# Performance work log

Hardware: AMD Instinct MI355X
Metric: run time of the kernel (lower is better)

## Reference

```python
import jax, jax.numpy as jnp
import numpy as np

S = 15      # subject_nums
C = 2048    # in_channels (extractor output dim)
NC = 3      # num_classes
B = 1024    # subject_batch_num (rows per subject)
SUBJ = 7    # target subject
KERNEL_MUL = 2.0
KERNEL_NUM = 5


def setup_inputs() -> dict:
    key = jax.random.key(0)
    k = jax.random.split(key, 5)
    x = jax.random.normal(k[0], (S * B, C), dtype=jnp.float32)
    labels = jax.random.randint(k[1], (S * B,), 0, NC)
    y = jax.nn.one_hot(labels, NC, dtype=jnp.float32)
    subject_label = jnp.repeat(jnp.arange(S, dtype=jnp.int32), B)
    W_add = 0.02 * jax.random.normal(k[2], (S, 512, C), dtype=jnp.float32)
    b_add = jnp.zeros((S, 512), dtype=jnp.float32)
    W_cls = 0.02 * jax.random.normal(k[3], (S, NC, 512), dtype=jnp.float32)
    b_cls = jnp.zeros((S, NC), dtype=jnp.float32)
    return {"x": x, "y": y, "subject_label": subject_label,
            "W_add": W_add, "b_add": b_add, "W_cls": W_cls, "b_cls": b_cls,
            "subject": SUBJ}


def _mmd(source, target):
    # Standard multi-kernel Gaussian MMD (DAN-style), as used in the repo.
    n = source.shape[0]
    total = jnp.concatenate([source, target], axis=0)      # [2n, d]
    sq = jnp.sum(total * total, axis=-1)
    d2 = sq[:, None] + sq[None, :] - 2.0 * (total @ total.T)  # [2n, 2n]
    m = 2 * n
    bandwidth = jnp.sum(d2) / (m * m - m)
    bandwidth = bandwidth / (KERNEL_MUL ** (KERNEL_NUM // 2))
    kernels = sum(jnp.exp(-d2 / (bandwidth * (KERNEL_MUL ** i))) for i in range(KERNEL_NUM))
    XX = kernels[:n, :n]
    YY = kernels[n:, n:]
    XY = kernels[:n, n:]
    YX = kernels[n:, :n]
    return jnp.mean(XX + YY - XY - YX)


def reference(x, y, subject_label, W_add, b_add, W_cls, b_cls, subject):
    S_ = W_add.shape[0]
    b = x.shape[0] // S_          # == (subject_label == subject).sum() by construction
    K = S_ - 1
    idx = np.array([i for i in range(S_) if i != subject])  # static: subject is a Python int

    xr = x.reshape(S_, b, -1)
    src = xr[idx]                 # [K, b, C] source-subject blocks
    tgt = xr[subject]             # [b, C] target-subject block
    Wk, bk = W_add[idx], b_add[idx]

    # Grouped per-subject addblock Linear(C -> 512)
    outs = jnp.einsum('kbc,kdc->kbd', src, Wk) + bk[:, None, :]       # [K, b, 512]
    t_outs = jnp.einsum('bc,kdc->kbd', tgt, Wk) + bk[:, None, :]      # [K, b, 512]

    # Class predictors: ReLU + Linear(512 -> NC), predictors 0..K-1 are used
    Wc, bc = W_cls[:K], b_cls[:K]
    logits = jnp.einsum('kbd,knd->kbn', jax.nn.relu(outs), Wc) + bc[:, None, :]
    t_logits = jnp.einsum('kbd,knd->kbn', jax.nn.relu(t_outs), Wc) + bc[:, None, :]

    # ---- MMD loss ----
    mmd_loss = jnp.mean(jax.vmap(_mmd)(outs, t_outs))

    # ---- DISC loss: pairwise |softmax - softmax| over source features ----
    P = jax.nn.softmax(outs, axis=-1)                                  # [K, b, 512]
    disc_loss = 0.0
    for i in range(K - 1):  # fixed small loop over subjects, inner term vectorized
        disc_loss = disc_loss + jnp.abs(P[i + 1:] - P[i]).mean(axis=(1, 2)).sum()
    disc_loss = disc_loss * 2.0 / (K * (K - 1))

    # ---- CLS loss: KL(one-hot/soft target || log_softmax(logits)) ----
    yr = y.reshape(S_, b, -1)[idx]                                     # [K, b, NC]
    logp = jax.nn.log_softmax(logits, axis=-1)
    safe_y = jnp.where(yr > 0, yr, 1.0)
    kl = jnp.where(yr > 0, yr * (jnp.log(safe_y) - logp), 0.0)         # 0*log0 -> 0 (torch kl_div)
    cls_loss = kl.sum(-1).mean()

    # ---- PRED ACC on target subject ----
    t_prob = jax.nn.softmax(t_logits, axis=-1).mean(axis=0)            # [b, NC]
    y_tgt = y.reshape(S_, b, -1)[subject]
    pred = jnp.sum(jnp.argmax(t_prob, axis=1) == jnp.argmax(y_tgt, axis=1))
    nums = b

    return (mmd_loss * 0.1, disc_loss * 0.4, cls_loss, pred, nums)
```

## Files before the change

kernel.cpp:

```cpp
#include <hip/hip_runtime.h>
#include <hip/hip_bf16.h>
#include <stdint.h>

typedef __attribute__((ext_vector_type(8))) __bf16 bf16x8;
typedef __attribute__((ext_vector_type(4))) float f32x4;

#define CDIM 2048
#define DDIM 512

__device__ __forceinline__ unsigned short f2bf(float f) {
  union { float f; unsigned u; } a; a.f = f;
  unsigned r = a.u + 0x7FFFu + ((a.u >> 16) & 1u);
  return (unsigned short)(r >> 16);
}
__device__ __forceinline__ float bf2f(unsigned short h) {
  union { unsigned u; float f; } a; a.u = ((unsigned)h) << 16;
  return a.f;
}

typedef const __attribute__((address_space(1))) void gas_void;
typedef __attribute__((address_space(3))) void las_void;
__device__ __forceinline__ void async16(const void* g, void* l) {
  __builtin_amdgcn_global_load_lds((gas_void*)g, (las_void*)l, 16, 0, 0);
}

__device__ __forceinline__ float blockSum256(float v) {
  __shared__ float sh[4];
  #pragma unroll
  for (int o = 32; o; o >>= 1) v += __shfl_xor(v, o, 64);
  int lane = threadIdx.x & 63, w = threadIdx.x >> 6;
  __syncthreads();
  if (lane == 0) sh[w] = v;
  __syncthreads();
  return sh[0] + sh[1] + sh[2] + sh[3];
}

__device__ __forceinline__ bf16x8 lds_frag(const unsigned short* base, int row, int cb) {
  return *(const bf16x8*)(base + row*64 + (((cb ^ (row & 7))) << 3));
}

__global__ __launch_bounds__(256) void k_convert(const float* __restrict__ x,
    const float* __restrict__ w, uint2* __restrict__ x16, uint2* __restrict__ w16) {
  const int nx4 = 15*1024*CDIM/4;
  const int nw4 = 15*DDIM*CDIM/4;
  int stride = gridDim.x * blockDim.x;
  for (int i = blockIdx.x*blockDim.x + threadIdx.x; i < nx4; i += stride) {
    float4 v = ((const float4*)x)[i];
    x16[i] = make_uint2((unsigned)f2bf(v.x) | ((unsigned)f2bf(v.y) << 16),
                        (unsigned)f2bf(v.z) | ((unsigned)f2bf(v.w) << 16));
  }
  for (int i = blockIdx.x*blockDim.x + threadIdx.x; i < nw4; i += stride) {
    float4 v = ((const float4*)w)[i];
    w16[i] = make_uint2((unsigned)f2bf(v.x) | ((unsigned)f2bf(v.y) << 16),
                        (unsigned)f2bf(v.z) | ((unsigned)f2bf(v.w) << 16));
  }
}

__global__ __launch_bounds__(256) void k_gemm1(
    const unsigned short* __restrict__ x16,
    const unsigned short* __restrict__ w16,
    const float* __restrict__ b_add,
    const int* __restrict__ subj_p,
    unsigned short* __restrict__ t16)
{
  const int subj = *subj_p;
  int bid = blockIdx.x;
  int k  = bid >> 6;
  int t  = bid & 63;
  int mt = t >> 2, nt = t & 3;
  int ik = (k < subj) ? k : (k + 1);

  __shared__ unsigned short As[128*64];
  __shared__ unsigned short Bs[128*64];

  int tid = threadIdx.x;
  int lane = tid & 63;
  int w = tid >> 6;
  int wm = w >> 1, wn = w & 1;
  int rlane = lane >> 3;
  int col8  = ((lane & 7) ^ rlane) << 3;

  const unsigned short* Bbase = w16 + (size_t)ik * DDIM * CDIM;

  f32x4 acc[4][4];
  #pragma unroll
  for (int a = 0; a < 4; a++)
    #pragma unroll
    for (int b = 0; b < 4; b++) acc[a][b] = f32x4{0.f,0.f,0.f,0.f};

  for (int ks = 0; ks < CDIM; ks += 64) {
    #pragma unroll
    for (int i = 0; i < 4; i++) {
      int c = w*4 + i;
      int r = c*8 + rlane;
      int gr = mt*128 + r;
      int xrow = ((gr < 1024) ? ik : subj) * 1024 + (gr & 1023);
      async16(x16 + (size_t)xrow*CDIM + ks + col8, (char*)As + c*1024);
      int gn = nt*128 + r;
      async16(Bbase + (size_t)gn*CDIM + ks + col8, (char*)Bs + c*1024);
    }
    __syncthreads();
    #pragma unroll
    for (int kk = 0; kk < 64; kk += 32) {
      bf16x8 af[4], bfr[4];
      #pragma unroll
      for (int a = 0; a < 4; a++)
        af[a] = lds_frag(As, wm*64 + a*16 + (lane & 15), (kk >> 3) + (lane >> 4));
      #pragma unroll
      for (int b = 0; b < 4; b++)
        bfr[b] = lds_frag(Bs, wn*64 + b*16 + (lane & 15), (kk >> 3) + (lane >> 4));
      #pragma unroll
      for (int a = 0; a < 4; a++)
        #pragma unroll
        for (int b = 0; b < 4; b++)
          acc[a][b] = __builtin_amdgcn_mfma_f32_16x16x32_bf16(af[a], bfr[b], acc[a][b], 0, 0, 0);
    }
    __syncthreads();
  }
  const float* bias = b_add + ik*DDIM;
  #pragma unroll
  for (int b = 0; b < 4; b++) {
    int coln = nt*128 + wn*64 + b*16 + (lane & 15);
    float bv = bias[coln];
    #pragma unroll
    for (int a = 0; a < 4; a++) {
      #pragma unroll
      for (int r = 0; r < 4; r++) {
        int rowm = mt*128 + wm*64 + a*16 + ((lane >> 4) << 2) + r;
        t16[((size_t)k*2048 + rowm)*DDIM + coln] = f2bf(acc[a][b][r] + bv);
      }
    }
  }
}

__global__ __launch_bounds__(256) void k_rowred(const unsigned short* __restrict__ t16,
    float* __restrict__ sq, float* __restrict__ rmax, float* __restrict__ rinv,
    float* __restrict__ scol)
{
  __shared__ float cs[4][512];
  int tidx = threadIdx.x;
  int w = tidx >> 6;
  int lane = tidx & 63;
  int wid = blockIdx.x*4 + w;
  int k = wid >> 11;
  uint4 v = *(const uint4*)(t16 + (size_t)wid * DDIM + lane*8);
  unsigned uu[4] = {v.x, v.y, v.z, v.w};
  float f[8];
  #pragma unroll
  for (int q = 0; q < 4; q++) {
    f[2*q]   = bf2f((unsigned short)(uu[q] & 0xffffu));
    f[2*q+1] = bf2f((unsigned short)(uu[q] >> 16));
  }
  float s2 = 0.f, mx = -3.4e38f;
  #pragma unroll
  for (int j = 0; j < 8; j++) { s2 += f[j]*f[j]; mx = fmaxf(mx, f[j]); }
  #pragma unroll
  for (int o = 32; o; o >>= 1) { s2 += __shfl_xor(s2, o, 64); mx = fmaxf(mx, __shfl_xor(mx, o, 64)); }
  float se = 0.f;
  #pragma unroll
  for (int j = 0; j < 8; j++) se += __expf(f[j] - mx);
  #pragma unroll
  for (int o = 32; o; o >>= 1) se += __shfl_xor(se, o, 64);
  if (lane == 0) { sq[wid] = s2; rmax[wid] = mx; rinv[wid] = 1.f/se; }
  #pragma unroll
  for (int j = 0; j < 8; j++) cs[w][lane*8 + j] = f[j];
  __syncthreads();
  atomicAdd(&scol[k*512 + tidx],       cs[0][tidx]     + cs[1][tidx]     + cs[2][tidx]     + cs[3][tidx]);
  atomicAdd(&scol[k*512 + 256 + tidx], cs[0][tidx+256] + cs[1][tidx+256] + cs[2][tidx+256] + cs[3][tidx+256]);
}

__global__ __launch_bounds__(256) void k_bw(const float* __restrict__ sq,
    const float* __restrict__ scol, float* __restrict__ c2)
{
  int k = blockIdx.x;
  float a = 0.f;
  for (int r = threadIdx.x; r < 2048; r += 256) a += sq[k*2048 + r];
  float b = 0.f;
  for (int d = threadIdx.x; d < 512; d += 256) { float v = scol[k*512 + d]; b += v*v; }
  float atot = blockSum256(a);
  float btot = blockSum256(b);
  if (threadIdx.x == 0) {
    float sumd2 = 2.f*2048.f*atot - 2.f*btot;
    float bw = sumd2 / (2048.f*2048.f - 2048.f) * 0.25f;
    #pragma unroll
    for (int i = 0; i < 5; i++)
      c2[k*5 + i] = -1.4426950408889634f / (bw * (float)(1 << i));
  }
}

__global__ __launch_bounds__(256) void k_mmd(
    const unsigned short* __restrict__ t16,
    const float* __restrict__ sq,
    const float* __restrict__ c2,
    float* __restrict__ g_acc)
{
  int bid = blockIdx.x;
  int k = bid / 136;
  int tri = bid - k*136;
  int it = 0;
  while (tri >= 16 - it) { tri -= 16 - it; it++; }
  int jt = it + tri;

  const unsigned short* T = t16 + (size_t)k * 2048 * DDIM;

  __shared__ unsigned short As[128*64];
  __shared__ unsigned short Bs[128*64];
  __shared__ float sqs[256];

  int tid = threadIdx.x;
  int lane = tid & 63;
  int w = tid >> 6;
  int wm = w >> 1, wn = w & 1;
  int rlane = lane >> 3;
  int col8  = ((lane & 7) ^ rlane) << 3;

  f32x4 acc[4][4];
  #pragma unroll
  for (int a = 0; a < 4; a++)
    #pragma unroll
    for (int b = 0; b < 4; b++) acc[a][b] = f32x4{0.f,0.f,0.f,0.f};

  for (int ks = 0; ks < DDIM; ks += 64) {
    #pragma unroll
    for (int i = 0; i < 4; i++) {
      int c = w*4 + i;
      int r = c*8 + rlane;
      async16(T + (size_t)(it*128 + r)*DDIM + ks + col8, (char*)As + c*1024);
      async16(T + (size_t)(jt*128 + r)*DDIM + ks + col8, (char*)Bs + c*1024);
    }
    __syncthreads();
    #pragma unroll
    for (int kk = 0; kk < 64; kk += 32) {
      bf16x8 af[4], bfr[4];
      #pragma unroll
      for (int a = 0; a < 4; a++)
        af[a] = lds_frag(As, wm*64 + a*16 + (lane & 15), (kk >> 3) + (lane >> 4));
      #pragma unroll
      for (int b = 0; b < 4; b++)
        bfr[b] = lds_frag(Bs, wn*64 + b*16 + (lane & 15), (kk >> 3) + (lane >> 4));
      #pragma unroll
      for (int a = 0; a < 4; a++)
        #pragma unroll
        for (int b = 0; b < 4; b++)
          acc[a][b] = __builtin_amdgcn_mfma_f32_16x16x32_bf16(af[a], bfr[b], acc[a][b], 0, 0, 0);
    }
    __syncthreads();
  }
  if (tid < 128) sqs[tid] = sq[k*2048 + it*128 + tid];
  else           sqs[tid] = sq[k*2048 + jt*128 + (tid - 128)];
  __syncthreads();

  float c0 = c2[k*5], c1 = c2[k*5+1], cA = c2[k*5+2], c3 = c2[k*5+3], c4 = c2[k*5+4];
  float part = 0.f;
  #pragma unroll
  for (int a = 0; a < 4; a++) {
    #pragma unroll
    for (int b = 0; b < 4; b++) {
      int rj = wn*64 + b*16 + (lane & 15);
      float sj = sqs[128 + rj];
      #pragma unroll
      for (int r = 0; r < 4; r++) {
        int ri = wm*64 + a*16 + ((lane >> 4) << 2) + r;
        float d2 = sqs[ri] + sj - 2.f*acc[a][b][r];
        part += exp2f(c0*d2) + exp2f(c1*d2) + exp2f(cA*d2) + exp2f(c3*d2) + exp2f(c4*d2);
      }
    }
  }
  float tot = blockSum256(part);
  if (tid == 0) {
    float sgn = ((it < 8) == (jt < 8)) ? 1.f : -1.f;
    float wgt = (it == jt) ? 1.f : 2.f;
    atomicAdd(&g_acc[k], sgn * wgt * tot);
  }
}

__global__ __launch_bounds__(256) void k_heads(const unsigned short* __restrict__ t16,
    const float* __restrict__ rmax, const float* __restrict__ rinv,
    const float* __restrict__ W_cls, const float* __restrict__ b_cls,
    const float* __restrict__ y, const int* __restrict__ subj_p,
    float* __restrict__ g_acc, float* __restrict__ pacc)
{
  if (blockIdx.x < 2048) {
    int b = blockIdx.x;
    int row = b >> 1;
    int d = ((b & 1) << 8) + threadIdx.x;
    float p[14];
    #pragma unroll
    for (int k = 0; k < 14; k++) {
      float tv = bf2f(t16[((size_t)(k*2048 + row))*DDIM + d]);
      p[k] = __expf(tv - rmax[k*2048 + row]) * rinv[k*2048 + row];
    }
    float s = 0.f;
    #pragma unroll
    for (int i2 = 0; i2 < 14; i2++)
      #pragma unroll
      for (int j2 = i2+1; j2 < 14; j2++)
        s += fabsf(p[i2] - p[j2]);
    float tot = blockSum256(s);
    if (threadIdx.x == 0) atomicAdd(&g_acc[14 + (b & 7)], tot);
  } else {
    __shared__ float shk[4];
    int bid = blockIdx.x - 2048;
    int w = threadIdx.x >> 6;
    int lane = threadIdx.x & 63;
    int wid = bid*4 + w;
    int k = wid >> 11, r = wid & 2047;
    uint4 v = *(const uint4*)(t16 + (size_t)wid * DDIM + lane*8);
    unsigned uu[4] = {v.x, v.y, v.z, v.w};
    float f[8];
    #pragma unroll
    for (int q = 0; q < 4; q++) {
      f[2*q]   = fmaxf(bf2f((unsigned short)(uu[q] & 0xffffu)), 0.f);
      f[2*q+1] = fmaxf(bf2f((unsigned short)(uu[q] >> 16)), 0.f);
    }
    const float* Wc = W_cls + k*3*DDIM;
    int d0 = lane*8;
    float l0 = 0.f, l1 = 0.f, l2 = 0.f;
    #pragma unroll
    for (int j = 0; j < 8; j++) {
      l0 += f[j]*Wc[d0+j];
      l1 += f[j]*Wc[DDIM + d0+j];
      l2 += f[j]*Wc[2*DDIM + d0+j];
    }
    #pragma unroll
    for (int o = 32; o; o >>= 1) {
      l0 += __shfl_xor(l0, o, 64); l1 += __shfl_xor(l1, o, 64); l2 += __shfl_xor(l2, o, 64);
    }
    if (r < 1024) {
      float kl = 0.f;
      if (lane == 0) {
        l0 += b_cls[k*3+0]; l1 += b_cls[k*3+1]; l2 += b_cls[k*3+2];
        float mx = fmaxf(l0, fmaxf(l1, l2));
        float lse = mx + __logf(__expf(l0-mx) + __expf(l1-mx) + __expf(l2-mx));
        int subj = *subj_p;
        int ik = (k < subj) ? k : k+1;
        const float* yr = y + ((size_t)(ik*1024 + r))*3;
        float tl = (yr[0] > 0.5f) ? l0 : ((yr[1] > 0.5f) ? l1 : l2);
        kl = lse - tl;
        shk[w] = kl;
      }
      __syncthreads();
      if (threadIdx.x == 0)
        atomicAdd(&g_acc[22 + k], shk[0] + shk[1] + shk[2] + shk[3]);
    } else {
      if (lane == 0) {
        l0 += b_cls[k*3+0]; l1 += b_cls[k*3+1]; l2 += b_cls[k*3+2];
        float mx = fmaxf(l0, fmaxf(l1, l2));
        float e0 = __expf(l0-mx), e1 = __expf(l1-mx), e2 = __expf(l2-mx);
        float inv = 1.f/(e0+e1+e2);
        int j = r - 1024;
        atomicAdd(&pacc[j*3 + 0], e0*inv);
        atomicAdd(&pacc[j*3 + 1], e1*inv);
        atomicAdd(&pacc[j*3 + 2], e2*inv);
      }
    }
  }
}

__global__ __launch_bounds__(256) void k_pred(const float* __restrict__ pacc,
    const float* __restrict__ y, const int* __restrict__ subj_p, float* __restrict__ g_acc)
{
  int j = blockIdx.x*256 + threadIdx.x;
  int subj = *subj_p;
  float p0 = pacc[j*3+0], p1 = pacc[j*3+1], p2 = pacc[j*3+2];
  int pa = 0; float pm = p0;
  if (p1 > pm) { pa = 1; pm = p1; }
  if (p2 > pm) { pa = 2; }
  const float* yt = y + ((size_t)(subj*1024 + j))*3;
  int ya = 0; float ym = yt[0];
  if (yt[1] > ym) { ya = 1; ym = yt[1]; }
  if (yt[2] > ym) { ya = 2; }
  float tot = blockSum256((pa == ya) ? 1.f : 0.f);
  if (threadIdx.x == 0) atomicAdd(&g_acc[36], tot);
}

__global__ void k_fin(const float* __restrict__ g_acc, float* __restrict__ out)
{
  if (threadIdx.x == 0 && blockIdx.x == 0) {
    float s = 0.f;
    for (int k = 0; k < 14; k++) s += g_acc[k];
    float disc = 0.f;
    for (int i = 14; i < 22; i++) disc += g_acc[i];
    float cls = 0.f;
    for (int i = 22; i < 36; i++) cls += g_acc[i];
    out[0] = 0.1f * s / (14.f * 1024.f * 1024.f);
    out[1] = 0.4f * disc * (2.f / (14.f*13.f)) / (1024.f*512.f);
    out[2] = cls / (14.f*1024.f);
    out[3] = g_acc[36];
    out[4] = 1024.f;
  }
}

extern "C" void kernel_launch(void* const* d_in, const int* in_sizes, int n_in,
                              void* d_out, int out_size, void* d_ws, size_t ws_size,
                              hipStream_t stream)
{
  (void)in_sizes; (void)n_in; (void)out_size; (void)ws_size;
  const float* x     = (const float*)d_in[0];
  const float* y     = (const float*)d_in[1];
  const float* W_add = (const float*)d_in[3];
  const float* b_add = (const float*)d_in[4];
  const float* W_cls = (const float*)d_in[5];
  const float* b_cls = (const float*)d_in[6];
  const int*   subj  = (const int*)d_in[7];

  char* ws = (char*)d_ws;
  size_t o = 0;
  auto take = [&](size_t b) { char* p = ws + o; o += (b + 255) & ~(size_t)255; return p; };
  unsigned short* X16 = (unsigned short*)take((size_t)15*1024*2048*2);
  unsigned short* W16 = (unsigned short*)take((size_t)15*512*2048*2);
  unsigned short* T16 = (unsigned short*)take((size_t)14*2048*512*2);
  float* SQ   = (float*)take((size_t)14*2048*4);
  float* RMAX = (float*)take((size_t)14*2048*4);
  float* RINV = (float*)take((size_t)14*2048*4);
  float* C2   = (float*)take(512);
  float* SCOL = (float*)take((size_t)14*512*4);
  float* PACC = (float*)take((size_t)1024*3*4);
  float* ACC  = (float*)take(256);

  hipMemsetAsync(SCOL, 0, 14*512*4 + 1024*3*4 + 256, stream);

  k_convert<<<2048, 256, 0, stream>>>(x, W_add, (uint2*)X16, (uint2*)W16);
  k_gemm1 <<<14*64, 256, 0, stream>>>(X16, W16, b_add, subj, T16);
  k_rowred<<<14*2048/4, 256, 0, stream>>>(T16, SQ, RMAX, RINV, SCOL);
  k_bw    <<<14, 256, 0, stream>>>(SQ, SCOL, C2);
  k_mmd   <<<14*136, 256, 0, stream>>>(T16, SQ, C2, ACC);
  k_heads <<<2048 + 14*2048/4, 256, 0, stream>>>(T16, RMAX, RINV, W_cls, b_cls, y, subj, ACC, PACC);
  k_pred  <<<4, 256, 0, stream>>>(PACC, y, subj, ACC);
  k_fin   <<<1, 64, 0, stream>>>(ACC, (float*)d_out);
}
```

Baseline: 527.5 us.

## Triple-buffer GEMM K-loops with async LDS loads and split column sums

Result: faster. 502.0 us (-4.8%).

```diff
diff --git a/kernel.cpp b/kernel.cpp
--- a/kernel.cpp
+++ b/kernel.cpp
@@ -23,6 +23,10 @@
 __device__ __forceinline__ void async16(const void* g, void* l) {
   __builtin_amdgcn_global_load_lds((gas_void*)g, (las_void*)l, 16, 0, 0);
 }
+
+#define VMW(n) asm volatile("s_waitcnt vmcnt(" #n ")" ::: "memory")
+#define SBAR() __builtin_amdgcn_s_barrier()
+#define SFENCE() __builtin_amdgcn_sched_barrier(0)
 
 __device__ __forceinline__ float blockSum256(float v) {
   __shared__ float sh[4];
@@ -56,7 +60,7 @@
   }
 }
 
-__global__ __launch_bounds__(256) void k_gemm1(
+__global__ __launch_bounds__(512, 2) void k_gemm1(
     const unsigned short* __restrict__ x16,
     const unsigned short* __restrict__ w16,
     const float* __restrict__ b_add,
@@ -65,22 +69,21 @@
 {
   const int subj = *subj_p;
   int bid = blockIdx.x;
-  int k  = bid >> 6;
-  int t  = bid & 63;
-  int mt = t >> 2, nt = t & 3;
+  int k  = bid >> 5;
+  int t  = bid & 31;
+  int mt = t >> 1, nt = t & 1;
   int ik = (k < subj) ? k : (k + 1);
 
-  __shared__ unsigned short As[128*64];
-  __shared__ unsigned short Bs[128*64];
+  __shared__ unsigned short lds[3*384*64];
 
   int tid = threadIdx.x;
   int lane = tid & 63;
   int w = tid >> 6;
-  int wm = w >> 1, wn = w & 1;
-  int rlane = lane >> 3;
-  int col8  = ((lane & 7) ^ rlane) << 3;
-
-  const unsigned short* Bbase = w16 + (size_t)ik * DDIM * CDIM;
+  int wm = w >> 2, wn = w & 3;
+  int rr = lane >> 3;
+  int cc8 = ((lane & 7) ^ rr) << 3;
+
+  const unsigned short* Bb = w16 + (size_t)ik * DDIM * CDIM;
 
   f32x4 acc[4][4];
   #pragma unroll
@@ -88,61 +91,87 @@
     #pragma unroll
     for (int b = 0; b < 4; b++) acc[a][b] = f32x4{0.f,0.f,0.f,0.f};
 
-  for (int ks = 0; ks < CDIM; ks += 64) {
+  auto stage = [&](int tt, int bufi) {
+    unsigned short* buf = lds + bufi*(384*64);
+    int ks = tt*64;
+    #pragma unroll
+    for (int i = 0; i < 2; i++) {
+      int r0 = (w*2 + i)*8;
+      int gr = mt*128 + r0 + rr;
+      int xrow = ((gr < 1024) ? ik : subj)*1024 + (gr & 1023);
+      async16(x16 + (size_t)xrow*CDIM + ks + cc8, buf + r0*64);
+    }
     #pragma unroll
     for (int i = 0; i < 4; i++) {
-      int c = w*4 + i;
-      int r = c*8 + rlane;
-      int gr = mt*128 + r;
-      int xrow = ((gr < 1024) ? ik : subj) * 1024 + (gr & 1023);
-      async16(x16 + (size_t)xrow*CDIM + ks + col8, (char*)As + c*1024);
-      int gn = nt*128 + r;
-      async16(Bbase + (size_t)gn*CDIM + ks + col8, (char*)Bs + c*1024);
-    }
-    __syncthreads();
-    #pragma unroll
-    for (int kk = 0; kk < 64; kk += 32) {
-      bf16x8 af[4], bfr[4];
-      #pragma unroll
-      for (int a = 0; a < 4; a++)
-        af[a] = lds_frag(As, wm*64 + a*16 + (lane & 15), (kk >> 3) + (lane >> 4));
-      #pragma unroll
-      for (int b = 0; b < 4; b++)
-        bfr[b] = lds_frag(Bs, wn*64 + b*16 + (lane & 15), (kk >> 3) + (lane >> 4));
-      #pragma unroll
-      for (int a = 0; a < 4; a++)
-        #pragma unroll
-        for (int b = 0; b < 4; b++)
-          acc[a][b] = __builtin_amdgcn_mfma_f32_16x16x32_bf16(af[a], bfr[b], acc[a][b], 0, 0, 0);
-    }
-    __syncthreads();
-  }
+      int r0 = (w*4 + i)*8;
+      int gn = nt*256 + r0 + rr;
+      async16(Bb + (size_t)gn*CDIM + ks + cc8, buf + 8192 + r0*64);
+    }
+  };
+
+  auto compute = [&](int bufi) {
+    const unsigned short* A = lds + bufi*(384*64);
+    const unsigned short* B = A + 8192;
+    bf16x8 af[4][2], bfr[4][2];
+    #pragma unroll
+    for (int a = 0; a < 4; a++)
+      #pragma unroll
+      for (int ksl = 0; ksl < 2; ksl++)
+        af[a][ksl] = lds_frag(A, wm*64 + a*16 + (lane & 15), ksl*4 + (lane >> 4));
+    #pragma unroll
+    for (int bb = 0; bb < 4; bb++)
+      #pragma unroll
+      for (int ksl = 0; ksl < 2; ksl++)
+        bfr[bb][ksl] = lds_frag(B, wn*64 + bb*16 + (lane & 15), ksl*4 + (lane >> 4));
+    __builtin_amdgcn_s_setprio(1);
+    #pragma unroll
+    for (int a = 0; a < 4; a++)
+      #pragma unroll
+      for (int bb = 0; bb < 4; bb++) {
+        acc[a][bb] = __builtin_amdgcn_mfma_f32_16x16x32_bf16(af[a][0], bfr[bb][0], acc[a][bb], 0, 0, 0);
+        acc[a][bb] = __builtin_amdgcn_mfma_f32_16x16x32_bf16(af[a][1], bfr[bb][1], acc[a][bb], 0, 0, 0);
+      }
+    __builtin_amdgcn_s_setprio(0);
+  };
+
+  stage(0, 0);
+  stage(1, 1);
+  VMW(6); SBAR(); SFENCE();
+
+  int cur = 0;
+  for (int tt = 0; tt < 30; ++tt) {
+    int nb = cur + 2; if (nb >= 3) nb -= 3;
+    stage(tt + 2, nb);
+    compute(cur);
+    VMW(6); SBAR(); SFENCE();
+    cur = (cur == 2) ? 0 : cur + 1;
+  }
+  compute(cur);
+  VMW(0); SBAR(); SFENCE();
+  cur = (cur == 2) ? 0 : cur + 1;
+  compute(cur);
+
   const float* bias = b_add + ik*DDIM;
   #pragma unroll
-  for (int b = 0; b < 4; b++) {
-    int coln = nt*128 + wn*64 + b*16 + (lane & 15);
+  for (int bb = 0; bb < 4; bb++) {
+    int coln = nt*256 + wn*64 + bb*16 + (lane & 15);
     float bv = bias[coln];
     #pragma unroll
     for (int a = 0; a < 4; a++) {
       #pragma unroll
       for (int r = 0; r < 4; r++) {
         int rowm = mt*128 + wm*64 + a*16 + ((lane >> 4) << 2) + r;
-        t16[((size_t)k*2048 + rowm)*DDIM + coln] = f2bf(acc[a][b][r] + bv);
+        t16[((size_t)k*2048 + rowm)*DDIM + coln] = f2bf(acc[a][bb][r] + bv);
       }
     }
   }
 }
 
 __global__ __launch_bounds__(256) void k_rowred(const unsigned short* __restrict__ t16,
-    float* __restrict__ sq, float* __restrict__ rmax, float* __restrict__ rinv,
-    float* __restrict__ scol)
-{
-  __shared__ float cs[4][512];
-  int tidx = threadIdx.x;
-  int w = tidx >> 6;
-  int lane = tidx & 63;
-  int wid = blockIdx.x*4 + w;
-  int k = wid >> 11;
+    float* __restrict__ sq, float* __restrict__ rmax, float* __restrict__ rinv)
+{
+  int wid = blockIdx.x*4 + (threadIdx.x >> 6);
+  int lane = threadIdx.x & 63;
   uint4 v = *(const uint4*)(t16 + (size_t)wid * DDIM + lane*8);
   unsigned uu[4] = {v.x, v.y, v.z, v.w};
   float f[8];
@@ -162,11 +191,19 @@
   #pragma unroll
   for (int o = 32; o; o >>= 1) se += __shfl_xor(se, o, 64);
   if (lane == 0) { sq[wid] = s2; rmax[wid] = mx; rinv[wid] = 1.f/se; }
-  #pragma unroll
-  for (int j = 0; j < 8; j++) cs[w][lane*8 + j] = f[j];
-  __syncthreads();
-  atomicAdd(&scol[k*512 + tidx],       cs[0][tidx]     + cs[1][tidx]     + cs[2][tidx]     + cs[3][tidx]);
-  atomicAdd(&scol[k*512 + 256 + tidx], cs[0][tidx+256] + cs[1][tidx+256] + cs[2][tidx+256] + cs[3][tidx+256]);
+}
+
+__global__ __launch_bounds__(256) void k_colsum(const unsigned short* __restrict__ t16,
+    float* __restrict__ scol)
+{
+  int b = blockIdx.x;
+  int k = b >> 4, sub = b & 15;
+  int d = ((sub & 1) << 8) + threadIdx.x;
+  int r0 = (sub >> 1) << 8;
+  const unsigned short* base = t16 + (size_t)k*2048*DDIM;
+  float s = 0.f;
+  for (int r = r0; r < r0 + 256; r++) s += bf2f(base[(size_t)r*DDIM + d]);
+  atomicAdd(&scol[k*DDIM + d], s);
 }
 
 __global__ __launch_bounds__(256) void k_bw(const float* __restrict__ sq,
@@ -188,7 +225,7 @@
   }
 }
 
-__global__ __launch_bounds__(256) void k_mmd(
+__global__ __launch_bounds__(256, 1) void k_mmd(
     const unsigned short* __restrict__ t16,
     const float* __restrict__ sq,
     const float* __restrict__ c2,
@@ -203,16 +240,15 @@
 
   const unsigned short* T = t16 + (size_t)k * 2048 * DDIM;
 
-  __shared__ unsigned short As[128*64];
-  __shared__ unsigned short Bs[128*64];
+  __shared__ unsigned short lds[3*256*64];
   __shared__ float sqs[256];
 
   int tid = threadIdx.x;
   int lane = tid & 63;
   int w = tid >> 6;
   int wm = w >> 1, wn = w & 1;
-  int rlane = lane >> 3;
-  int col8  = ((lane & 7) ^ rlane) << 3;
+  int rr = lane >> 3;
+  int cc8 = ((lane & 7) ^ rr) << 3;
 
   f32x4 acc[4][4];
   #pragma unroll
@@ -220,32 +256,63 @@
     #pragma unroll
     for (int b = 0; b < 4; b++) acc[a][b] = f32x4{0.f,0.f,0.f,0.f};
 
-  for (int ks = 0; ks < DDIM; ks += 64) {
+  auto stage = [&](int tt, int bufi) {
+    unsigned short* buf = lds + bufi*(256*64);
+    int ks = tt*64;
     #pragma unroll
     for (int i = 0; i < 4; i++) {
-      int c = w*4 + i;
-      int r = c*8 + rlane;
-      async16(T + (size_t)(it*128 + r)*DDIM + ks + col8, (char*)As + c*1024);
-      async16(T + (size_t)(jt*128 + r)*DDIM + ks + col8, (char*)Bs + c*1024);
-    }
-    __syncthreads();
-    #pragma unroll
-    for (int kk = 0; kk < 64; kk += 32) {
-      bf16x8 af[4], bfr[4];
-      #pragma unroll
-      for (int a = 0; a < 4; a++)
-        af[a] = lds_frag(As, wm*64 + a*16 + (lane & 15), (kk >> 3) + (lane >> 4));
-      #pragma unroll
-      for (int b = 0; b < 4; b++)
-        bfr[b] = lds_frag(Bs, wn*64 + b*16 + (lane & 15), (kk >> 3) + (lane >> 4));
-      #pragma unroll
-      for (int a = 0; a < 4; a++)
-        #pragma unroll
-        for (int b = 0; b < 4; b++)
-          acc[a][b] = __builtin_amdgcn_mfma_f32_16x16x32_bf16(af[a], bfr[b], acc[a][b], 0, 0, 0);
-    }
-    __syncthreads();
-  }
+      int r0 = (w*4 + i)*8;
+      async16(T + (size_t)(it*128 + r0 + rr)*DDIM + ks + cc8, buf + r0*64);
+    }
+    #pragma unroll
+    for (int i = 0; i < 4; i++) {
+      int r0 = (w*4 + i)*8;
+      async16(T + (size_t)(jt*128 + r0 + rr)*DDIM + ks + cc8, buf + 8192 + r0*64);
+    }
+  };
+
+  auto compute = [&](int bufi) {
+    const unsigned short* A = lds + bufi*(256*64);
+    const unsigned short* B = A + 8192;
+    bf16x8 af[4][2], bfr[4][2];
+    #pragma unroll
+    for (int a = 0; a < 4; a++)
+      #pragma unroll
+      for (int ksl = 0; ksl < 2; ksl++)
+        af[a][ksl] = lds_frag(A, wm*64 + a*16 + (lane & 15), ksl*4 + (lane >> 4));
+    #pragma unroll
+    for (int bb = 0; bb < 4; bb++)
+      #pragma unroll
+      for (int ksl = 0; ksl < 2; ksl++)
+        bfr[bb][ksl] = lds_frag(B, wn*64 + bb*16 + (lane & 15), ksl*4 + (lane >> 4));
+    __builtin_amdgcn_s_setprio(1);
+    #pragma unroll
+    for (int a = 0; a < 4; a++)
+      #pragma unroll
+      for (int bb = 0; bb < 4; bb++) {
+        acc[a][bb] = __builtin_amdgcn_mfma_f32_16x16x32_bf16(af[a][0], bfr[bb][0], acc[a][bb], 0, 0, 0);
+        acc[a][bb] = __builtin_amdgcn_mfma_f32_16x16x32_bf16(af[a][1], bfr[bb][1], acc[a][bb], 0, 0, 0);
+      }
+    __builtin_amdgcn_s_setprio(0);
+  };
+
+  stage(0, 0);
+  stage(1, 1);
+  VMW(8); SBAR(); SFENCE();
+
+  int cur = 0;
+  for (int tt = 0; tt < 6; ++tt) {
+    int nb = cur + 2; if (nb >= 3) nb -= 3;
+    stage(tt + 2, nb);
+    compute(cur);
+    VMW(8); SBAR(); SFENCE();
+    cur = (cur == 2) ? 0 : cur + 1;
+  }
+  compute(cur);
+  VMW(0); SBAR(); SFENCE();
+  cur = (cur == 2) ? 0 : cur + 1;
+  compute(cur);
+
   if (tid < 128) sqs[tid] = sq[k*2048 + it*128 + tid];
   else           sqs[tid] = sq[k*2048 + jt*128 + (tid - 128)];
   __syncthreads();
@@ -255,13 +322,13 @@
   #pragma unroll
   for (int a = 0; a < 4; a++) {
     #pragma unroll
-    for (int b = 0; b < 4; b++) {
-      int rj = wn*64 + b*16 + (lane & 15);
+    for (int bb = 0; bb < 4; bb++) {
+      int rj = wn*64 + bb*16 + (lane & 15);
       float sj = sqs[128 + rj];
       #pragma unroll
       for (int r = 0; r < 4; r++) {
         int ri = wm*64 + a*16 + ((lane >> 4) << 2) + r;
-        float d2 = sqs[ri] + sj - 2.f*acc[a][b][r];
+        float d2 = sqs[ri] + sj - 2.f*acc[a][bb][r];
         part += exp2f(c0*d2) + exp2f(c1*d2) + exp2f(cA*d2) + exp2f(c3*d2) + exp2f(c4*d2);
       }
     }
@@ -327,7 +394,6 @@
       l0 += __shfl_xor(l0, o, 64); l1 += __shfl_xor(l1, o, 64); l2 += __shfl_xor(l2, o, 64);
     }
     if (r < 1024) {
-      float kl = 0.f;
       if (lane == 0) {
         l0 += b_cls[k*3+0]; l1 += b_cls[k*3+1]; l2 += b_cls[k*3+2];
         float mx = fmaxf(l0, fmaxf(l1, l2));
@@ -336,8 +402,7 @@
         int ik = (k < subj) ? k : k+1;
         const float* yr = y + ((size_t)(ik*1024 + r))*3;
         float tl = (yr[0] > 0.5f) ? l0 : ((yr[1] > 0.5f) ? l1 : l2);
-        kl = lse - tl;
-        shk[w] = kl;
+        shk[w] = lse - tl;
       }
       __syncthreads();
       if (threadIdx.x == 0)
@@ -421,8 +486,9 @@
   hipMemsetAsync(SCOL, 0, 14*512*4 + 1024*3*4 + 256, stream);
 
   k_convert<<<2048, 256, 0, stream>>>(x, W_add, (uint2*)X16, (uint2*)W16);
-  k_gemm1 <<<14*64, 256, 0, stream>>>(X16, W16, b_add, subj, T16);
-  k_rowred<<<14*2048/4, 256, 0, stream>>>(T16, SQ, RMAX, RINV, SCOL);
+  k_gemm1 <<<14*32, 512, 0, stream>>>(X16, W16, b_add, subj, T16);
+  k_rowred<<<14*2048/4, 256, 0, stream>>>(T16, SQ, RMAX, RINV);
+  k_colsum<<<14*16, 256, 0, stream>>>(T16, SCOL);
   k_bw    <<<14, 256, 0, stream>>>(SQ, SCOL, C2);
   k_mmd   <<<14*136, 256, 0, stream>>>(T16, SQ, C2, ACC);
   k_heads <<<2048 + 14*2048/4, 256, 0, stream>>>(T16, RMAX, RINV, W_cls, b_cls, y, subj, ACC, PACC);
```
